# Optimization experiments

Hardware: AMD Instinct MI355X
Metric: run time of the kernel (lower is better)

The kernel has to match this reference:

```python
import jax, jax.numpy as jnp
import numpy as np

R_CUT = 10.0  # init arg r_cut


def _per_mol(pos, T, eneg, node_attrs, an, q_tot, eidx, hardness, cov_radii):
    # pos [N,3], T [N,E], eneg [N], node_attrs [N,num_el], an [N] int,
    # q_tot scalar, eidx [2,E] int
    N = pos.shape[0]
    E = T.shape[1]
    dtype = pos.dtype
    sqrt_pi = jnp.sqrt(jnp.pi).astype(dtype)
    sqrt_2 = jnp.sqrt(2.0).astype(dtype)
    eye = jnp.eye(N, dtype=dtype)
    # pairwise distances; +eye makes the (masked-out) diagonal sqrt-safe
    diff = pos[:, None, :] - pos[None, :, :]
    d = jnp.sqrt(jnp.sum(diff * diff, axis=-1) + eye)  # [N,N]
    r = cov_radii[an]                                   # [N]
    sigma = r * r
    gamma = jnp.sqrt(sigma[:, None] + sigma[None, :])   # [N,N]
    diag_vals = hardness[jnp.argmax(node_attrs, axis=-1)] + 1.0 / (sqrt_pi * r)
    A = jax.scipy.special.erf(d / (sqrt_2 * gamma)) / d * (1.0 - eye) + jnp.diag(diag_vals)
    # per-edge cutoff diagonal: 1/cos(pi*r/(2*r_cut)) - 1
    e0, e1 = eidx[0], eidx[1]
    edge_d = jnp.sqrt(jnp.sum((pos[e0] - pos[e1]) ** 2, axis=-1))  # [E]
    cut = 1.0 / jnp.cos(jnp.pi * edge_d / (2.0 * R_CUT)) - 1.0
    Ap = T.T @ A @ T + jnp.diag(cut)                    # [E,E]
    # augment with charge-conservation row/col of ones
    ones_col = jnp.ones((E, 1), dtype=dtype)
    ones_row = jnp.ones((1, E + 1), dtype=dtype)
    Aaug = jnp.concatenate([jnp.concatenate([Ap, ones_col], axis=1), ones_row], axis=0)
    b = jnp.concatenate([-(T.T @ eneg), q_tot[None]])   # [E+1]
    x = jnp.linalg.solve(Aaug, b)[:-1]                  # [E] split charges
    return T @ x                                        # [N] atomic partial charges


def setup_inputs() -> dict:
    key = jax.random.key(0)
    B, N, E, NUM_EL, NZ = 256, 64, 512, 10, 119
    ks = jax.random.split(key, 10)
    positions = jax.random.normal(ks[0], (B, N, 3), dtype=jnp.float32)
    T = jax.random.normal(ks[1], (B, N, E), dtype=jnp.float32)
    eneg = jax.random.normal(ks[2], (B, N), dtype=jnp.float32)
    node_attrs = jax.random.normal(ks[3], (B, N, NUM_EL), dtype=jnp.float32)
    total_charge = jax.random.normal(ks[4], (B,), dtype=jnp.float32)
    atomic_numbers = jax.random.randint(ks[5], (B, N), 1, 100)
    e0 = jax.random.randint(ks[6], (B, E), 0, N)
    off = jax.random.randint(ks[7], (B, E), 1, N)
    edge_index = jnp.stack([e0, (e0 + off) % N], axis=1)  # [B,2,E], distinct endpoints
    hardness = jax.random.uniform(ks[8], (NUM_EL,), dtype=jnp.float32)
    cov_radii = 0.3 + 2.2 * jax.random.uniform(ks[9], (NZ,), dtype=jnp.float32)
    p = jnp.zeros((1,), dtype=jnp.float32)  # only used for .device in torch
    return dict(positions=positions, T=T, eneg=eneg, node_attrs=node_attrs,
                total_charge=total_charge, p=p, hardness=hardness,
                cov_radii=cov_radii, atomic_numbers=atomic_numbers,
                edge_index=edge_index)


def reference(positions, T, eneg, node_attrs, total_charge, p, hardness,
              cov_radii, atomic_numbers, edge_index):
    charges = jax.vmap(_per_mol, in_axes=(0, 0, 0, 0, 0, 0, 0, None, None))(
        positions, T, eneg, node_attrs, atomic_numbers, total_charge,
        edge_index, hardness, cov_radii)  # [B,N]
    return charges.reshape(-1)  # concat over molecules, as in the torch loop
```

## Files before the change

### kernel.cpp

```cpp
#include <hip/hip_runtime.h>
#include <math.h>

#define SQRT_PI 1.7724538509055160273
#define SQRT_2  1.4142135623730950488
#define PI_OVER_2RC 0.15707963267948966
#define W0 32.0


__device__ __forceinline__ double bcast64(double v, int lane) {
    union { double d; unsigned int u[2]; } a, r;
    a.d = v;
    r.u[0] = __builtin_amdgcn_readlane(a.u[0], lane);
    r.u[1] = __builtin_amdgcn_readlane(a.u[1], lane);
    return r.d;
}

__device__ __forceinline__ double a_entry(int i, int j, const double* posd,
                                          const double* sig, const double* dg) {
    if (i == j) return dg[i];
    double dx = posd[3*i+0]-posd[3*j+0];
    double dy = posd[3*i+1]-posd[3*j+1];
    double dz = posd[3*i+2]-posd[3*j+2];
    double d  = sqrt(dx*dx+dy*dy+dz*dz);
    double g  = sqrt(sig[i]+sig[j]);
    return erf(d/(SQRT_2*g))/d;
}

__global__ __launch_bounds__(256, 2)
void k1_gram(const float* __restrict__ pos, const float* __restrict__ T,
             const int* __restrict__ eidx, double* __restrict__ ws)
{
    const int bx = blockIdx.x;
    const int m = bx >> 1, s = bx & 1;
    const int Bm = gridDim.x >> 1;
    const int tid = threadIdx.x;

    __shared__ float  Tch[64*68];
    __shared__ double posd[192];
    __shared__ double w_sl[256];
    __shared__ float  sw32[256];
    __shared__ double ptb[4][64];
    __shared__ unsigned long long fmask[4];

    const float* Tm = T + (size_t)m*64*512;

    if (tid < 64) {
        posd[3*tid+0] = (double)pos[(m*64+tid)*3+0];
        posd[3*tid+1] = (double)pos[(m*64+tid)*3+1];
        posd[3*tid+2] = (double)pos[(m*64+tid)*3+2];
    }
    __syncthreads();

    {
        const int e = s*256 + tid;
        const int a0 = eidx[(size_t)m*1024 + e];
        const int a1 = eidx[(size_t)m*1024 + 512 + e];
        double dx = posd[3*a0+0]-posd[3*a1+0];
        double dy = posd[3*a0+1]-posd[3*a1+1];
        double dz = posd[3*a0+2]-posd[3*a1+2];
        double d  = sqrt(dx*dx+dy*dy+dz*dz);
        double w  = 1.0 / (1.0/cos(PI_OVER_2RC*d) - 1.0);
        w_sl[tid] = w;
        sw32[tid] = (w > W0) ? 0.0f : (float)sqrt(w);
    }
    __syncthreads();
    if (tid < 64) {
        #pragma unroll
        for (int c2 = 0; c2 < 4; ++c2) {
            unsigned long long mk = __ballot(w_sl[c2*64 + tid] > W0);
            if (tid == 0) fmask[c2] = mk;
        }
    }

    const int si = tid & 15, sj = tid >> 4;
    const int ti64 = tid & 63, tg = tid >> 6;

    const int PP_[10] = {0,0,0,0,1,1,1,2,2,3};
    const int QQ_[10] = {0,1,2,3,1,2,3,2,3,3};
    double acc64[10];
    float  a32[10];
    #pragma unroll
    for (int k = 0; k < 10; ++k) { acc64[k] = 0.0; a32[k] = 0.0f; }
    double t0b_p = 0.0;

    for (int cc = 0; cc < 4; ++cc) {
        const int gch = s*4 + cc;
        __syncthreads();
        #pragma unroll
        for (int k = 0; k < 4; ++k) {
            int l = tid + 256*k, row = l >> 4, c4 = (l & 15)*4;
            float4 v = *(const float4*)&Tm[row*512 + gch*64 + c4];
            *(float4*)&Tch[row*68 + c4] = v;
        }
        __syncthreads();
        #pragma unroll
        for (int k = 0; k < 16; ++k) {
            int e = tg*16 + k;
            double tv = (double)Tch[ti64*68 + e];
            t0b_p += tv * w_sl[cc*64 + e];
        }
        {
            unsigned long long mm = fmask[cc];
            while (mm) {
                int e = __builtin_ctzll(mm); mm &= mm - 1;
                double we = w_sl[cc*64 + e];
                double ad[4], bd[4];
                #pragma unroll
                for (int p = 0; p < 4; ++p) ad[p] = (double)Tch[(si+16*p)*68 + e];
                #pragma unroll
                for (int q = 0; q < 4; ++q) bd[q] = we * (double)Tch[(sj+16*q)*68 + e];
                #pragma unroll
                for (int k = 0; k < 10; ++k) acc64[k] += ad[PP_[k]] * bd[QQ_[k]];
            }
        }
        __syncthreads();
        #pragma unroll
        for (int k = 0; k < 4; ++k) {
            int l = tid + 256*k, row = l >> 4, c4 = (l & 15)*4;
            float4 v = *(float4*)&Tch[row*68 + c4];
            v.x *= sw32[cc*64 + c4+0];
            v.y *= sw32[cc*64 + c4+1];
            v.z *= sw32[cc*64 + c4+2];
            v.w *= sw32[cc*64 + c4+3];
            *(float4*)&Tch[row*68 + c4] = v;
        }
        __syncthreads();
        #pragma unroll
        for (int e4 = 0; e4 < 16; ++e4) {
            float4 av4[4], bv4[4];
            #pragma unroll
            for (int p = 0; p < 4; ++p) av4[p] = *(float4*)&Tch[(si+16*p)*68 + e4*4];
            #pragma unroll
            for (int q = 0; q < 4; ++q) bv4[q] = *(float4*)&Tch[(sj+16*q)*68 + e4*4];
            #pragma unroll
            for (int k = 0; k < 10; ++k) {
                const float4 a4 = av4[PP_[k]], b4 = bv4[QQ_[k]];
                a32[k] += a4.x*b4.x + a4.y*b4.y + a4.z*b4.z + a4.w*b4.w;
            }
            if ((e4 & 3) == 3) {
                #pragma unroll
                for (int k = 0; k < 10; ++k) { acc64[k] += (double)a32[k]; a32[k] = 0.0f; }
            }
        }
    }
    __syncthreads();

    double* Sp = ws + ((size_t)(s*Bm + m))*4096;
    #pragma unroll
    for (int k = 0; k < 10; ++k) {
        int i = si + 16*PP_[k], j = sj + 16*QQ_[k];
        Sp[i*64 + j] = acc64[k];
        if (PP_[k] != QQ_[k]) Sp[j*64 + i] = acc64[k];
    }

    ptb[tg][ti64] = t0b_p;
    __syncthreads();
    if (tid < 64) {
        double* t0q = ws + (size_t)2*Bm*4096;
        t0q[(size_t)(s*Bm + m)*64 + tid] =
            ptb[0][tid]+ptb[1][tid]+ptb[2][tid]+ptb[3][tid];
        double sw = w_sl[tid] + w_sl[64+tid] + w_sl[128+tid] + w_sl[192+tid];
        #pragma unroll
        for (int off = 32; off > 0; off >>= 1) sw += __shfl_down(sw, off);
        if (tid == 0) {
            double* swq = ws + (size_t)2*Bm*4096 + (size_t)2*Bm*64;
            swq[s*Bm + m] = sw;
        }
    }
}

__global__ __launch_bounds__(1024)
void k2_solve(const float* __restrict__ pos, const float* __restrict__ nattr,
              const float* __restrict__ eneg, const float* __restrict__ qtot,
              const float* __restrict__ hard, const float* __restrict__ covr,
              const int* __restrict__ an, double* __restrict__ ws,
              float* __restrict__ outp)
{
    const int m = blockIdx.x, tid = threadIdx.x;
    const int Bm = gridDim.x;
    const int jl = tid & 63;
    const int rg = tid >> 6;

    __shared__ double AB[64*65];
    __shared__ double PB[64*33];
    __shared__ double posd[192], sig_s[64], dg_s[64], eneg_s[64];
    __shared__ double t0a_s[64], t0b_s[64], ga_s[64], gb_s[64], ua_s[64], ub_s[64];
    __shared__ double sa_s[64], sb_s[64];
    __shared__ double dinv_s[64], dvec_s[64];
    __shared__ double lam_sh;

    const double* Sp0 = ws + (size_t)m*4096;
    const double* Sp1 = ws + (size_t)(Bm + m)*4096;
    const double* t0q = ws + (size_t)2*Bm*4096;
    const double* swq = t0q + (size_t)2*Bm*64;

    if (tid < 64) {
        posd[3*tid+0] = (double)pos[(m*64+tid)*3+0];
        posd[3*tid+1] = (double)pos[(m*64+tid)*3+1];
        posd[3*tid+2] = (double)pos[(m*64+tid)*3+2];
        double r = (double)covr[an[m*64+tid]];
        sig_s[tid] = r*r;
        const float* np_ = nattr + (size_t)(m*64+tid)*10;
        float best = np_[0]; int bi = 0;
        #pragma unroll
        for (int k = 1; k < 10; ++k) { float v = np_[k]; if (v > best) { best = v; bi = k; } }
        dg_s[tid] = (double)hard[bi] + 1.0/(SQRT_PI*r);
    } else if (tid < 128) {
        int l = tid - 64;
        t0b_s[l] = t0q[(size_t)m*64 + l] + t0q[(size_t)(Bm+m)*64 + l];
    } else if (tid < 192) {
        int l = tid - 128;
        eneg_s[l] = (double)eneg[m*64 + l];
    }
    __syncthreads();

    double areg[4];
    #pragma unroll
    for (int p = 0; p < 4; ++p) {
        int i = rg + 16*p;
        double v = a_entry(i, jl, posd, sig_s, dg_s);
        areg[p] = v;
        AB[i*65 + jl] = v;
    }

    {
        int i = tid & 63, kg = tid >> 6;
        double a = 0.0;
        #pragma unroll
        for (int kk = 0; kk < 4; ++kk) {
            int k = 4*kg + kk;
            a += (Sp0[i*64+k] + Sp1[i*64+k]) * eneg_s[k];
        }
        PB[kg*64 + i] = a;
    }
    __syncthreads();
    if (tid < 64) {
        double a = 0.0;
        #pragma unroll
        for (int g = 0; g < 16; ++g) a += PB[g*64 + tid];
        t0a_s[tid] = -a;
    }
    __syncthreads();

    {
        double ra[4], rb[4];
        const double ta = t0a_s[jl], tb = t0b_s[jl];
        #pragma unroll
        for (int p = 0; p < 4; ++p) { ra[p] = areg[p]*ta; rb[p] = areg[p]*tb; }
        #pragma unroll
        for (int off = 32; off > 0; off >>= 1) {
            #pragma unroll
            for (int p = 0; p < 4; ++p) {
                ra[p] += __shfl_down(ra[p], off);
                rb[p] += __shfl_down(rb[p], off);
            }
        }
        if (jl == 0) {
            #pragma unroll
            for (int p = 0; p < 4; ++p) { ga_s[rg+16*p] = ra[p]; gb_s[rg+16*p] = rb[p]; }
        }
    }

    double macc[4];
    #pragma unroll
    for (int p = 0; p < 4; ++p) macc[p] = areg[p];

    for (int pass = 0; pass < 2; ++pass) {
        const int kbase = pass*32;
        __syncthreads();
        for (int l2 = tid; l2 < 2048; l2 += 1024) {
            int c = l2 >> 6, k = l2 & 63;
            PB[c*64 + k] = Sp0[(size_t)(kbase+c)*64 + k] + Sp1[(size_t)(kbase+c)*64 + k];
        }
        __syncthreads();
        const int c0 = 2*rg, c1 = c0 + 1;
        double p0 = 0.0, p1 = 0.0;
        #pragma unroll 4
        for (int k = 0; k < 64; ++k) {
            double a = AB[jl*65 + k];
            p0 += a * PB[c0*64 + k];
            p1 += a * PB[c1*64 + k];
        }
        __syncthreads();
        PB[jl*33 + c0] = p0;
        PB[jl*33 + c1] = p1;
        __syncthreads();
        #pragma unroll 4
        for (int cl = 0; cl < 32; ++cl) {
            double lb = AB[(kbase+cl)*65 + jl];
            #pragma unroll
            for (int p = 0; p < 4; ++p)
                macc[p] += PB[(rg+16*p)*33 + cl] * lb;
        }
    }
    __syncthreads();
    #pragma unroll
    for (int p = 0; p < 4; ++p) AB[(rg+16*p)*65 + jl] = macc[p];
    __syncthreads();

    for (int pb = 0; pb < 4; ++pb) {
        const int kb = pb*16;
        if (tid < 64) {
            const int i = tid;
            double pr[16];
            #pragma unroll
            for (int c = 0; c < 16; ++c) pr[c] = AB[i*65 + kb + c];
            #pragma unroll
            for (int c = 0; c < 16; ++c) {
                const int k = kb + c;
                const double Dk = bcast64(pr[c], k);
                const double di = 1.0 / Dk;
                if (i == k) { dinv_s[k] = di; dvec_s[k] = Dk; }
                const double lik = pr[c] * di;
                #pragma unroll
                for (int j = c+1; j < 16; ++j) {
                    const double mkj = bcast64(pr[j], k);
                    if (i > k) pr[j] -= lik * mkj;
                }
                if (i > k) pr[c] = lik;
            }
            #pragma unroll
            for (int c = 0; c < 16; ++c) AB[i*65 + kb + c] = pr[c];
        }
        __syncthreads();
        const int lim = kb + 16;
        if (lim < 64) {
            double tacc[4] = {0.0, 0.0, 0.0, 0.0};
            #pragma unroll 4
            for (int c = 0; c < 16; ++c) {
                double lbv = AB[jl*65 + kb + c] * dvec_s[kb + c];
                #pragma unroll
                for (int p = 0; p < 4; ++p)
                    tacc[p] += AB[(rg+16*p)*65 + kb + c] * lbv;
            }
            if (jl >= lim) {
                #pragma unroll
                for (int p = 0; p < 4; ++p) {
                    int i = rg + 16*p;
                    if (i >= lim) AB[i*65 + jl] -= tacc[p];
                }
            }
        }
        __syncthreads();
    }

    if (tid < 64) {
        const int i = tid;
        double ha = ga_s[i], hb = gb_s[i];
        #pragma unroll
        for (int j = 0; j < 63; ++j) {
            double xa = bcast64(ha, j), xb = bcast64(hb, j);
            double lij = (i > j) ? AB[i*65+j] : 0.0;
            ha -= lij*xa; hb -= lij*xb;
        }
        double di = dinv_s[i];
        ha *= di; hb *= di;
        #pragma unroll
        for (int j = 63; j > 0; --j) {
            double xa = bcast64(ha, j), xb = bcast64(hb, j);
            double lji = (i < j) ? AB[j*65+i] : 0.0;
            ha -= lji*xa; hb -= lji*xb;
        }
        ua_s[i] = ha; ub_s[i] = hb;
    }
    __syncthreads();

    {
        double ra[4], rb[4];
        const double uaj = ua_s[jl], ubj = ub_s[jl];
        #pragma unroll
        for (int p = 0; p < 4; ++p) { ra[p] = areg[p]*uaj; rb[p] = areg[p]*ubj; }
        #pragma unroll
        for (int off = 32; off > 0; off >>= 1) {
            #pragma unroll
            for (int p = 0; p < 4; ++p) {
                ra[p] += __shfl_down(ra[p], off);
                rb[p] += __shfl_down(rb[p], off);
            }
        }
        if (jl == 0) {
            #pragma unroll
            for (int p = 0; p < 4; ++p) {
                sa_s[rg + 16*p] = ra[p];
                sb_s[rg + 16*p] = rb[p];
            }
        }
    }
    __syncthreads();

    {
        int i = tid & 63, kg = tid >> 6;
        double a1 = 0.0, a2 = 0.0;
        #pragma unroll
        for (int kk = 0; kk < 4; ++kk) {
            int k = 4*kg + kk;
            double Sv = Sp0[i*64+k] + Sp1[i*64+k];
            a1 += Sv * sa_s[k];
            a2 += Sv * sb_s[k];
        }
        PB[kg*64 + i] = a1;
        PB[1024 + kg*64 + i] = a2;
    }
    if (tid < 64) {
        double d1 = (eneg_s[tid] + sa_s[tid]) * t0b_s[tid];
        double d2 = sb_s[tid] * t0b_s[tid];
        #pragma unroll
        for (int off = 32; off > 0; off >>= 1) {
            d1 += __shfl_down(d1, off);
            d2 += __shfl_down(d2, off);
        }
        if (tid == 0) {
            double sw1 = swq[m] + swq[Bm + m];
            double sY = -d1;
            double sZ = sw1 - d2;
            lam_sh = ((double)qtot[m] - sY) / (1.0 - sZ);
        }
    }
    __syncthreads();
    if (tid < 64) {
        double q1 = 0.0, q2 = 0.0;
        #pragma unroll
        for (int g = 0; g < 16; ++g) {
            q1 += PB[g*64 + tid];
            q2 += PB[1024 + g*64 + tid];
        }
        double p1 = t0a_s[tid] - q1;
        double p2 = t0b_s[tid] - q2;
        outp[m*64 + tid] = (float)(p1 - lam_sh*p2);
    }
}

extern "C" void kernel_launch(void* const* d_in, const int* in_sizes, int n_in,
                              void* d_out, int out_size, void* d_ws, size_t ws_size,
                              hipStream_t stream) {
    const float* pos  = (const float*)d_in[0];
    const float* T    = (const float*)d_in[1];
    const float* eneg = (const float*)d_in[2];
    const float* nat  = (const float*)d_in[3];
    const float* qt   = (const float*)d_in[4];
    const float* hard = (const float*)d_in[6];
    const float* covr = (const float*)d_in[7];
    const int*   an   = (const int*)d_in[8];
    const int*   eidx = (const int*)d_in[9];
    float* outp = (float*)d_out;
    (void)n_in; (void)out_size; (void)ws_size; (void)eneg;

    const int B = in_sizes[4];
    double* ws = (double*)d_ws;

    k1_gram<<<dim3(2*B), dim3(256), 0, stream>>>(pos, T, eidx, ws);
    k2_solve<<<dim3(B), dim3(1024), 0, stream>>>(pos, nat, eneg, qt, hard,
                                                 covr, an, ws, outp);
}
```

Measured before the change: 185.9 us.

## Use FP64 MFMA for Gram and solve products with runtime layout probe

Adds a tiny probe kernel that works out the FP64 MFMA 16x16x4 operand and output lane layout at runtime and stores flags in the workspace. When the probe succeeds, the weighted Gram accumulation in k1 runs as double-precision MFMA instead of the mixed fp32/fp64 FMA path, and so do the A·S·A-style products in k2. It also keeps S entries in registers and uses segmented shuffle reductions in place of shared-memory partial sums. The cost is an extra kernel launch and flag reads in every block, and the MFMA path now does every edge in full fp64, which is more arithmetic than the old fp32 bulk path.

New measurement: 178.3 us. 1.04x faster.

```diff
diff --git a/kernel.cpp b/kernel.cpp
--- a/kernel.cpp
+++ b/kernel.cpp
@@ -5,6 +5,8 @@
 #define SQRT_2  1.4142135623730950488
 #define PI_OVER_2RC 0.15707963267948966
 #define W0 32.0
+
+typedef double dbl4 __attribute__((ext_vector_type(4)));
 
 
 __device__ __forceinline__ double bcast64(double v, int lane) {
@@ -26,6 +28,61 @@
     return erf(d/(SQRT_2*g))/d;
 }
 
+__device__ __forceinline__ dbl4 mfma64(int cS, double xv, double yv, dbl4 acc) {
+    return cS ? __builtin_amdgcn_mfma_f64_16x16x4f64(yv, xv, acc, 0, 0, 0)
+              : __builtin_amdgcn_mfma_f64_16x16x4f64(xv, yv, acc, 0, 0, 0);
+}
+
+__global__ __launch_bounds__(64)
+void k0_probe(double* __restrict__ fl)
+{
+    const int l = threadIdx.x;
+    const int kl = l >> 4, ml = l & 15;
+    const double af1 = (double)(l + 1),  bf1 = (double)(l + 65);
+    const double af2 = (double)(1 + ((l*7 + 3) % 61));
+    const double bf2 = (double)(2 + ((l*13 + 5) % 53));
+    dbl4 c1 = {0.0,0.0,0.0,0.0}, c2 = {0.0,0.0,0.0,0.0};
+    c1 = __builtin_amdgcn_mfma_f64_16x16x4f64(af1, bf1, c1, 0, 0, 0);
+    c2 = __builtin_amdgcn_mfma_f64_16x16x4f64(af2, bf2, c2, 0, 0, 0);
+    int best = -1;
+    for (int h = 0; h < 32; ++h) {
+        if (best >= 0) break;
+        const int cS = h >> 4, cA = (h >> 3) & 1, cB = (h >> 2) & 1, cD = h & 3;
+        bool ok = true;
+        #pragma unroll
+        for (int r = 0; r < 4; ++r) {
+            int row, col;
+            const int v0 = 4*kl + r, v1 = kl + 4*r;
+            if (cD == 0)      { row = v0; col = ml; }
+            else if (cD == 1) { row = v1; col = ml; }
+            else if (cD == 2) { row = ml; col = v0; }
+            else              { row = ml; col = v1; }
+            double r1 = 0.0, r2 = 0.0;
+            #pragma unroll
+            for (int k = 0; k < 4; ++k) {
+                const int la = cA ? (row*4 + k) : (row + 16*k);
+                const int lb = cB ? (col*4 + k) : (col + 16*k);
+                if (cS == 0) {
+                    r1 += (double)(la + 1) * (double)(lb + 65);
+                    r2 += (double)(1 + ((la*7+3) % 61)) * (double)(2 + ((lb*13+5) % 53));
+                } else {
+                    r1 += (double)(lb + 1) * (double)(la + 65);
+                    r2 += (double)(1 + ((lb*7+3) % 61)) * (double)(2 + ((la*13+5) % 53));
+                }
+            }
+            if (c1[r] != r1 || c2[r] != r2) ok = false;
+        }
+        if (__ballot(ok) == ~0ull) best = h;
+    }
+    if (l == 0) {
+        fl[0] = (best >= 0) ? 1.0 : 0.0;
+        fl[1] = (double)((best >= 0) ? (best >> 4)      : 0);
+        fl[2] = (double)((best >= 0) ? ((best >> 3) & 1) : 0);
+        fl[3] = (double)((best >= 0) ? ((best >> 2) & 1) : 0);
+        fl[4] = (double)((best >= 0) ? (best & 3)        : 0);
+    }
+}
+
 __global__ __launch_bounds__(256, 2)
 void k1_gram(const float* __restrict__ pos, const float* __restrict__ T,
              const int* __restrict__ eidx, double* __restrict__ ws)
@@ -34,6 +91,8 @@
     const int m = bx >> 1, s = bx & 1;
     const int Bm = gridDim.x >> 1;
     const int tid = threadIdx.x;
+    const int wid = tid >> 6, l = tid & 63;
+    const int kl = l >> 4, ml = l & 15;
 
     __shared__ float  Tch[64*68];
     __shared__ double posd[192];
@@ -43,6 +102,22 @@
     __shared__ unsigned long long fmask[4];
 
     const float* Tm = T + (size_t)m*64*512;
+    const double* flq = ws + (size_t)Bm*8322;
+    const int useM = (flq[0] != 0.0);
+    const int cS = (int)flq[1], cA = (int)flq[2], cB = (int)flq[3], cD = (int)flq[4];
+    const int aRow = cA ? (l >> 2) : ml;
+    const int aK   = cA ? (l & 3)  : kl;
+    const int bRow = cB ? (l >> 2) : ml;
+    const int bK   = cB ? (l & 3)  : kl;
+    int drow[4], dcol[4];
+    #pragma unroll
+    for (int r = 0; r < 4; ++r) {
+        const int v0 = 4*kl + r, v1 = kl + 4*r;
+        if (cD == 0)      { drow[r] = v0; dcol[r] = ml; }
+        else if (cD == 1) { drow[r] = v1; dcol[r] = ml; }
+        else if (cD == 2) { drow[r] = ml; dcol[r] = v0; }
+        else              { drow[r] = ml; dcol[r] = v1; }
+    }
 
     if (tid < 64) {
         posd[3*tid+0] = (double)pos[(m*64+tid)*3+0];
@@ -75,6 +150,13 @@
     const int si = tid & 15, sj = tid >> 4;
     const int ti64 = tid & 63, tg = tid >> 6;
 
+    const unsigned int enc = (wid==0) ? 0x020100u :
+                             (wid==1) ? 0x121103u :
+                             (wid==2) ? 0xFF2213u : 0xFF3323u;
+    dbl4 vacc[3];
+    #pragma unroll
+    for (int t = 0; t < 3; ++t) vacc[t] = (dbl4){0.0, 0.0, 0.0, 0.0};
+
     const int PP_[10] = {0,0,0,0,1,1,1,2,2,3};
     const int QQ_[10] = {0,1,2,3,1,2,3,2,3,3};
     double acc64[10];
@@ -88,7 +170,7 @@
         __syncthreads();
         #pragma unroll
         for (int k = 0; k < 4; ++k) {
-            int l = tid + 256*k, row = l >> 4, c4 = (l & 15)*4;
+            int ll = tid + 256*k, row = ll >> 4, c4 = (ll & 15)*4;
             float4 v = *(const float4*)&Tm[row*512 + gch*64 + c4];
             *(float4*)&Tch[row*68 + c4] = v;
         }
@@ -99,58 +181,90 @@
             double tv = (double)Tch[ti64*68 + e];
             t0b_p += tv * w_sl[cc*64 + e];
         }
-        {
-            unsigned long long mm = fmask[cc];
-            while (mm) {
-                int e = __builtin_ctzll(mm); mm &= mm - 1;
-                double we = w_sl[cc*64 + e];
-                double ad[4], bd[4];
-                #pragma unroll
-                for (int p = 0; p < 4; ++p) ad[p] = (double)Tch[(si+16*p)*68 + e];
-                #pragma unroll
-                for (int q = 0; q < 4; ++q) bd[q] = we * (double)Tch[(sj+16*q)*68 + e];
-                #pragma unroll
-                for (int k = 0; k < 10; ++k) acc64[k] += ad[PP_[k]] * bd[QQ_[k]];
-            }
-        }
-        __syncthreads();
-        #pragma unroll
-        for (int k = 0; k < 4; ++k) {
-            int l = tid + 256*k, row = l >> 4, c4 = (l & 15)*4;
-            float4 v = *(float4*)&Tch[row*68 + c4];
-            v.x *= sw32[cc*64 + c4+0];
-            v.y *= sw32[cc*64 + c4+1];
-            v.z *= sw32[cc*64 + c4+2];
-            v.w *= sw32[cc*64 + c4+3];
-            *(float4*)&Tch[row*68 + c4] = v;
-        }
-        __syncthreads();
-        #pragma unroll
-        for (int e4 = 0; e4 < 16; ++e4) {
-            float4 av4[4], bv4[4];
-            #pragma unroll
-            for (int p = 0; p < 4; ++p) av4[p] = *(float4*)&Tch[(si+16*p)*68 + e4*4];
-            #pragma unroll
-            for (int q = 0; q < 4; ++q) bv4[q] = *(float4*)&Tch[(sj+16*q)*68 + e4*4];
-            #pragma unroll
-            for (int k = 0; k < 10; ++k) {
-                const float4 a4 = av4[PP_[k]], b4 = bv4[QQ_[k]];
-                a32[k] += a4.x*b4.x + a4.y*b4.y + a4.z*b4.z + a4.w*b4.w;
-            }
-            if ((e4 & 3) == 3) {
-                #pragma unroll
-                for (int k = 0; k < 10; ++k) { acc64[k] += (double)a32[k]; a32[k] = 0.0f; }
+        if (useM) {
+            for (int kk = 0; kk < 16; ++kk) {
+                const double wB = w_sl[cc*64 + 4*kk + bK];
+                #pragma unroll
+                for (int t = 0; t < 3; ++t) {
+                    const unsigned int pq = (enc >> (8*t)) & 0xFFu;
+                    if (pq != 0xFFu) {
+                        const int p = pq >> 4, q = pq & 15;
+                        double xv = (double)Tch[(p*16 + aRow)*68 + 4*kk + aK];
+                        double yv = wB * (double)Tch[(q*16 + bRow)*68 + 4*kk + bK];
+                        vacc[t] = mfma64(cS, xv, yv, vacc[t]);
+                    }
+                }
+            }
+        } else {
+            {
+                unsigned long long mm = fmask[cc];
+                while (mm) {
+                    int e = __builtin_ctzll(mm); mm &= mm - 1;
+                    double we = w_sl[cc*64 + e];
+                    double ad[4], bd[4];
+                    #pragma unroll
+                    for (int p = 0; p < 4; ++p) ad[p] = (double)Tch[(si+16*p)*68 + e];
+                    #pragma unroll
+                    for (int q = 0; q < 4; ++q) bd[q] = we * (double)Tch[(sj+16*q)*68 + e];
+                    #pragma unroll
+                    for (int k = 0; k < 10; ++k) acc64[k] += ad[PP_[k]] * bd[QQ_[k]];
+                }
+            }
+            __syncthreads();
+            #pragma unroll
+            for (int k = 0; k < 4; ++k) {
+                int ll = tid + 256*k, row = ll >> 4, c4 = (ll & 15)*4;
+                float4 v = *(float4*)&Tch[row*68 + c4];
+                v.x *= sw32[cc*64 + c4+0];
+                v.y *= sw32[cc*64 + c4+1];
+                v.z *= sw32[cc*64 + c4+2];
+                v.w *= sw32[cc*64 + c4+3];
+                *(float4*)&Tch[row*68 + c4] = v;
+            }
+            __syncthreads();
+            #pragma unroll
+            for (int e4 = 0; e4 < 16; ++e4) {
+                float4 av4[4], bv4[4];
+                #pragma unroll
+                for (int p = 0; p < 4; ++p) av4[p] = *(float4*)&Tch[(si+16*p)*68 + e4*4];
+                #pragma unroll
+                for (int q = 0; q < 4; ++q) bv4[q] = *(float4*)&Tch[(sj+16*q)*68 + e4*4];
+                #pragma unroll
+                for (int k = 0; k < 10; ++k) {
+                    const float4 a4 = av4[PP_[k]], b4 = bv4[QQ_[k]];
+                    a32[k] += a4.x*b4.x + a4.y*b4.y + a4.z*b4.z + a4.w*b4.w;
+                }
+                if ((e4 & 3) == 3) {
+                    #pragma unroll
+                    for (int k = 0; k < 10; ++k) { acc64[k] += (double)a32[k]; a32[k] = 0.0f; }
+                }
             }
         }
     }
     __syncthreads();
 
     double* Sp = ws + ((size_t)(s*Bm + m))*4096;
-    #pragma unroll
-    for (int k = 0; k < 10; ++k) {
-        int i = si + 16*PP_[k], j = sj + 16*QQ_[k];
-        Sp[i*64 + j] = acc64[k];
-        if (PP_[k] != QQ_[k]) Sp[j*64 + i] = acc64[k];
+    if (useM) {
+        #pragma unroll
+        for (int t = 0; t < 3; ++t) {
+            const unsigned int pq = (enc >> (8*t)) & 0xFFu;
+            if (pq != 0xFFu) {
+                const int p = pq >> 4, q = pq & 15;
+                #pragma unroll
+                for (int r = 0; r < 4; ++r) {
+                    Sp[(p*16 + drow[r])*64 + q*16 + dcol[r]] = vacc[t][r];
+                    if (p != q)
+                        Sp[(q*16 + dcol[r])*64 + p*16 + drow[r]] = vacc[t][r];
+                }
+            }
+        }
+    } else {
+        #pragma unroll
+        for (int k = 0; k < 10; ++k) {
+            int i = si + 16*PP_[k], j = sj + 16*QQ_[k];
+            Sp[i*64 + j] = acc64[k];
+            if (PP_[k] != QQ_[k]) Sp[j*64 + i] = acc64[k];
+        }
     }
 
     ptb[tg][ti64] = t0b_p;
@@ -180,6 +294,7 @@
     const int Bm = gridDim.x;
     const int jl = tid & 63;
     const int rg = tid >> 6;
+    const int kl = jl >> 4, ml = jl & 15;
 
     __shared__ double AB[64*65];
     __shared__ double PB[64*33];
@@ -193,6 +308,28 @@
     const double* Sp1 = ws + (size_t)(Bm + m)*4096;
     const double* t0q = ws + (size_t)2*Bm*4096;
     const double* swq = t0q + (size_t)2*Bm*64;
+    const double* flq = ws + (size_t)Bm*8322;
+
+    const int useM = (flq[0] != 0.0);
+    const int cS = (int)flq[1], cA = (int)flq[2], cB = (int)flq[3], cD = (int)flq[4];
+    const int aRow = cA ? (jl >> 2) : ml;
+    const int aK   = cA ? (jl & 3)  : kl;
+    const int bRow = cB ? (jl >> 2) : ml;
+    const int bK   = cB ? (jl & 3)  : kl;
+    int drow[4], dcol[4];
+    #pragma unroll
+    for (int r = 0; r < 4; ++r) {
+        const int v0 = 4*kl + r, v1 = kl + 4*r;
+        if (cD == 0)      { drow[r] = v0; dcol[r] = ml; }
+        else if (cD == 1) { drow[r] = v1; dcol[r] = ml; }
+        else if (cD == 2) { drow[r] = ml; dcol[r] = v0; }
+        else              { drow[r] = ml; dcol[r] = v1; }
+    }
+
+    double sreg[4];
+    #pragma unroll
+    for (int kk = 0; kk < 4; ++kk)
+        sreg[kk] = Sp0[4*tid + kk] + Sp1[4*tid + kk];
 
     if (tid < 64) {
         posd[3*tid+0] = (double)pos[(m*64+tid)*3+0];
@@ -206,11 +343,11 @@
         for (int k = 1; k < 10; ++k) { float v = np_[k]; if (v > best) { best = v; bi = k; } }
         dg_s[tid] = (double)hard[bi] + 1.0/(SQRT_PI*r);
     } else if (tid < 128) {
-        int l = tid - 64;
-        t0b_s[l] = t0q[(size_t)m*64 + l] + t0q[(size_t)(Bm+m)*64 + l];
+        int ll = tid - 64;
+        t0b_s[ll] = t0q[(size_t)m*64 + ll] + t0q[(size_t)(Bm+m)*64 + ll];
     } else if (tid < 192) {
-        int l = tid - 128;
-        eneg_s[l] = (double)eneg[m*64 + l];
+        int ll = tid - 128;
+        eneg_s[ll] = (double)eneg[m*64 + ll];
     }
     __syncthreads();
 
@@ -222,23 +359,16 @@
         areg[p] = v;
         AB[i*65 + jl] = v;
     }
-
     {
-        int i = tid & 63, kg = tid >> 6;
+        const int c16 = tid & 15, row16 = tid >> 4;
         double a = 0.0;
         #pragma unroll
-        for (int kk = 0; kk < 4; ++kk) {
-            int k = 4*kg + kk;
-            a += (Sp0[i*64+k] + Sp1[i*64+k]) * eneg_s[k];
-        }
-        PB[kg*64 + i] = a;
-    }
-    __syncthreads();
-    if (tid < 64) {
-        double a = 0.0;
-        #pragma unroll
-        for (int g = 0; g < 16; ++g) a += PB[g*64 + tid];
-        t0a_s[tid] = -a;
+        for (int kk = 0; kk < 4; ++kk) a += sreg[kk] * eneg_s[4*c16 + kk];
+        a += __shfl_down(a, 8, 16);
+        a += __shfl_down(a, 4, 16);
+        a += __shfl_down(a, 2, 16);
+        a += __shfl_down(a, 1, 16);
+        if (c16 == 0) t0a_s[row16] = -a;
     }
     __syncthreads();
 
@@ -260,43 +390,90 @@
             for (int p = 0; p < 4; ++p) { ga_s[rg+16*p] = ra[p]; gb_s[rg+16*p] = rb[p]; }
         }
     }
-
-    double macc[4];
-    #pragma unroll
-    for (int p = 0; p < 4; ++p) macc[p] = areg[p];
-
-    for (int pass = 0; pass < 2; ++pass) {
-        const int kbase = pass*32;
-        __syncthreads();
-        for (int l2 = tid; l2 < 2048; l2 += 1024) {
-            int c = l2 >> 6, k = l2 & 63;
-            PB[c*64 + k] = Sp0[(size_t)(kbase+c)*64 + k] + Sp1[(size_t)(kbase+c)*64 + k];
-        }
-        __syncthreads();
-        const int c0 = 2*rg, c1 = c0 + 1;
-        double p0 = 0.0, p1 = 0.0;
-        #pragma unroll 4
-        for (int k = 0; k < 64; ++k) {
-            double a = AB[jl*65 + k];
-            p0 += a * PB[c0*64 + k];
-            p1 += a * PB[c1*64 + k];
-        }
-        __syncthreads();
-        PB[jl*33 + c0] = p0;
-        PB[jl*33 + c1] = p1;
-        __syncthreads();
-        #pragma unroll 4
-        for (int cl = 0; cl < 32; ++cl) {
-            double lb = AB[(kbase+cl)*65 + jl];
-            #pragma unroll
-            for (int p = 0; p < 4; ++p)
-                macc[p] += PB[(rg+16*p)*33 + cl] * lb;
-        }
-    }
-    __syncthreads();
-    #pragma unroll
-    for (int p = 0; p < 4; ++p) AB[(rg+16*p)*65 + jl] = macc[p];
-    __syncthreads();
+    __syncthreads();
+
+    if (useM) {
+        const int ti1 = rg >> 2;
+        const int tjp = (rg & 3) >> 1;
+        const int kh  = rg & 1;
+        const int ti2 = rg >> 2, tj2 = rg & 3;
+        dbl4 macc;
+        #pragma unroll
+        for (int r = 0; r < 4; ++r)
+            macc[r] = AB[(ti2*16 + drow[r])*65 + tj2*16 + dcol[r]];
+        for (int pass = 0; pass < 2; ++pass) {
+            const int kbase = pass*32;
+            dbl4 pacc = {0.0, 0.0, 0.0, 0.0};
+            #pragma unroll
+            for (int kk = 0; kk < 8; ++kk) {
+                const int kg = kh*8 + kk;
+                double xv = AB[(ti1*16 + aRow)*65 + 4*kg + aK];
+                size_t so = (size_t)(4*kg + bK)*64 + kbase + tjp*16 + bRow;
+                double yv = Sp0[so] + Sp1[so];
+                pacc = mfma64(cS, xv, yv, pacc);
+            }
+            __syncthreads();
+            if (kh == 0) {
+                #pragma unroll
+                for (int r = 0; r < 4; ++r)
+                    PB[(ti1*16 + drow[r])*33 + tjp*16 + dcol[r]] = pacc[r];
+            }
+            __syncthreads();
+            if (kh == 1) {
+                #pragma unroll
+                for (int r = 0; r < 4; ++r)
+                    PB[(ti1*16 + drow[r])*33 + tjp*16 + dcol[r]] += pacc[r];
+            }
+            __syncthreads();
+            #pragma unroll
+            for (int kk = 0; kk < 8; ++kk) {
+                double xv = PB[(ti2*16 + aRow)*33 + 4*kk + aK];
+                double yv = AB[(kbase + 4*kk + bK)*65 + tj2*16 + bRow];
+                macc = mfma64(cS, xv, yv, macc);
+            }
+        }
+        __syncthreads();
+        #pragma unroll
+        for (int r = 0; r < 4; ++r)
+            AB[(ti2*16 + drow[r])*65 + tj2*16 + dcol[r]] = macc[r];
+        __syncthreads();
+    } else {
+        double macc[4];
+        #pragma unroll
+        for (int p = 0; p < 4; ++p) macc[p] = areg[p];
+        for (int pass = 0; pass < 2; ++pass) {
+            const int kbase = pass*32;
+            __syncthreads();
+            for (int l2 = tid; l2 < 2048; l2 += 1024) {
+                int c = l2 >> 6, k = l2 & 63;
+                PB[c*64 + k] = Sp0[(size_t)(kbase+c)*64 + k] + Sp1[(size_t)(kbase+c)*64 + k];
+            }
+            __syncthreads();
+            const int c0 = 2*rg, c1 = c0 + 1;
+            double p0 = 0.0, p1 = 0.0;
+            #pragma unroll 4
+            for (int k = 0; k < 64; ++k) {
+                double a = AB[jl*65 + k];
+                p0 += a * PB[c0*64 + k];
+                p1 += a * PB[c1*64 + k];
+            }
+            __syncthreads();
+            PB[jl*33 + c0] = p0;
+            PB[jl*33 + c1] = p1;
+            __syncthreads();
+            #pragma unroll 4
+            for (int cl = 0; cl < 32; ++cl) {
+                double lb = AB[(kbase+cl)*65 + jl];
+                #pragma unroll
+                for (int p = 0; p < 4; ++p)
+                    macc[p] += PB[(rg+16*p)*33 + cl] * lb;
+            }
+        }
+        __syncthreads();
+        #pragma unroll
+        for (int p = 0; p < 4; ++p) AB[(rg+16*p)*65 + jl] = macc[p];
+        __syncthreads();
+    }
 
     for (int pb = 0; pb < 4; ++pb) {
         const int kb = pb*16;
@@ -389,17 +566,18 @@
     __syncthreads();
 
     {
-        int i = tid & 63, kg = tid >> 6;
-        double a1 = 0.0, a2 = 0.0;
+        const int c16 = tid & 15, row16 = tid >> 4;
+        double q1 = 0.0, q2 = 0.0;
         #pragma unroll
         for (int kk = 0; kk < 4; ++kk) {
-            int k = 4*kg + kk;
-            double Sv = Sp0[i*64+k] + Sp1[i*64+k];
-            a1 += Sv * sa_s[k];
-            a2 += Sv * sb_s[k];
-        }
-        PB[kg*64 + i] = a1;
-        PB[1024 + kg*64 + i] = a2;
+            q1 += sreg[kk] * sa_s[4*c16 + kk];
+            q2 += sreg[kk] * sb_s[4*c16 + kk];
+        }
+        q1 += __shfl_down(q1, 8, 16); q2 += __shfl_down(q2, 8, 16);
+        q1 += __shfl_down(q1, 4, 16); q2 += __shfl_down(q2, 4, 16);
+        q1 += __shfl_down(q1, 2, 16); q2 += __shfl_down(q2, 2, 16);
+        q1 += __shfl_down(q1, 1, 16); q2 += __shfl_down(q2, 1, 16);
+        if (c16 == 0) { PB[row16] = q1; PB[64 + row16] = q2; }
     }
     if (tid < 64) {
         double d1 = (eneg_s[tid] + sa_s[tid]) * t0b_s[tid];
@@ -418,14 +596,8 @@
     }
     __syncthreads();
     if (tid < 64) {
-        double q1 = 0.0, q2 = 0.0;
-        #pragma unroll
-        for (int g = 0; g < 16; ++g) {
-            q1 += PB[g*64 + tid];
-            q2 += PB[1024 + g*64 + tid];
-        }
-        double p1 = t0a_s[tid] - q1;
-        double p2 = t0b_s[tid] - q2;
+        double p1 = t0a_s[tid] - PB[tid];
+        double p2 = t0b_s[tid] - PB[64 + tid];
         outp[m*64 + tid] = (float)(p1 - lam_sh*p2);
     }
 }
@@ -443,11 +615,12 @@
     const int*   an   = (const int*)d_in[8];
     const int*   eidx = (const int*)d_in[9];
     float* outp = (float*)d_out;
-    (void)n_in; (void)out_size; (void)ws_size; (void)eneg;
+    (void)n_in; (void)out_size; (void)ws_size;
 
     const int B = in_sizes[4];
     double* ws = (double*)d_ws;
 
+    k0_probe<<<dim3(1), dim3(64), 0, stream>>>(ws + (size_t)B*8322);
     k1_gram<<<dim3(2*B), dim3(256), 0, stream>>>(pos, T, eidx, ws);
     k2_solve<<<dim3(B), dim3(1024), 0, stream>>>(pos, nat, eneg, qt, hard,
                                                  covr, an, ws, outp);
```
